# Kernel tuning notes

Measured on AMD Instinct MI355X. Metric: run time of the kernel, lower is better.

The kernel has to match this reference:

```python
import jax, jax.numpy as jnp
import numpy as np

B, T, D = 2, 2048, 1024
NH, DH = 16, 64  # inner = NH*DH = D
SCALE_INIT = 0.02


def setup_inputs() -> dict:
    key = jax.random.key(0)
    kx, kq, kk, kv, ko = jax.random.split(key, 5)
    return {
        "x": jax.random.normal(kx, (B, T, D), dtype=jnp.float32),
        "Wq": jax.random.normal(kq, (D, NH * DH), dtype=jnp.float32) * SCALE_INIT,
        "Wk": jax.random.normal(kk, (D, NH * DH), dtype=jnp.float32) * SCALE_INIT,
        "Wv": jax.random.normal(kv, (D, NH * DH), dtype=jnp.float32) * SCALE_INIT,
        "Wo": jax.random.normal(ko, (NH * DH, D), dtype=jnp.float32) * SCALE_INIT,
    }


def reference(x, Wq, Wk, Wv, Wo):
    # x: (B, T, D)
    b, t, _ = x.shape

    def split_heads(h):
        # (B, T, NH*DH) -> (B, NH, T, DH)
        return h.reshape(b, t, NH, DH).transpose(0, 2, 1, 3)

    q = split_heads(x @ Wq)
    k = split_heads(x @ Wk)
    v = split_heads(x @ Wv)

    scale = jnp.asarray(1.0 / np.sqrt(DH), dtype=x.dtype)
    # The per-chunk loop in the original is mathematically equivalent to
    # full causal attention: each query row attends to keys with k_pos <= q_pos.
    scores = jnp.einsum("bhqd,bhkd->bhqk", q, k) * scale  # (B, NH, T, T)
    causal_mask = jnp.arange(t)[None, :] > jnp.arange(t)[:, None]  # k_pos > q_pos
    scores = jnp.where(causal_mask, -jnp.inf, scores)
    attn = jax.nn.softmax(scores, axis=-1)
    attn = jnp.nan_to_num(attn)  # matches torch.nan_to_num (no fully-masked rows in causal case)
    o = jnp.einsum("bhqk,bhkd->bhqd", attn, v)  # (B, NH, T, DH)
    o = o.transpose(0, 2, 1, 3).reshape(b, t, NH * DH)  # merge heads
    return o @ Wo  # (B, T, D)
```

## Files before the change

### kernel.cpp

```cpp
#include <hip/hip_runtime.h>
#include <hip/hip_bf16.h>
#include <string.h>

#define Bsz 2
#define Tsz 2048
#define Dsz 1024
#define NHsz 16
#define Msz (Bsz*Tsz)

typedef unsigned short bfu;
typedef __attribute__((ext_vector_type(8))) short short8;
typedef __attribute__((ext_vector_type(4))) short short4v;
typedef __attribute__((ext_vector_type(4))) float floatx4;

__device__ __forceinline__ bfu f2bf(float f) {
  unsigned int u = __builtin_bit_cast(unsigned int, f);
  u += 0x7fffu + ((u >> 16) & 1u);
  return (bfu)(u >> 16);
}

__device__ __forceinline__ float fexp2(float x) {
#if __has_builtin(__builtin_amdgcn_exp2f)
  return __builtin_amdgcn_exp2f(x);
#else
  return exp2f(x);
#endif
}

__device__ __forceinline__ short4v pack4bf(float a, float b, float c_, float d) {
  __hip_bfloat162 h01 = __float22bfloat162_rn(make_float2(a, b));
  __hip_bfloat162 h23 = __float22bfloat162_rn(make_float2(c_, d));
  uint2 uu;
  memcpy(&uu.x, &h01, 4);
  memcpy(&uu.y, &h23, 4);
  return __builtin_bit_cast(short4v, uu);
}

__device__ __forceinline__ short8 pack8bf(float4 a, float4 b) {
  __hip_bfloat162 h0 = __float22bfloat162_rn(make_float2(a.x, a.y));
  __hip_bfloat162 h1 = __float22bfloat162_rn(make_float2(a.z, a.w));
  __hip_bfloat162 h2 = __float22bfloat162_rn(make_float2(b.x, b.y));
  __hip_bfloat162 h3 = __float22bfloat162_rn(make_float2(b.z, b.w));
  uint4 u;
  memcpy(&u.x, &h0, 4); memcpy(&u.y, &h1, 4);
  memcpy(&u.z, &h2, 4); memcpy(&u.w, &h3, 4);
  return __builtin_bit_cast(short8, u);
}

__device__ __forceinline__ void async16(const void* g, void* l) {
  void* gnc = (void*)g;
  __builtin_amdgcn_global_load_lds((__attribute__((address_space(1))) void*)gnc,
                                   (__attribute__((address_space(3))) void*)l,
                                   16, 0, 0);
}

__global__ __launch_bounds__(256) void transpose_w(const float* __restrict__ W0, const float* __restrict__ W1,
                                                   const float* __restrict__ W2, const float* __restrict__ W3,
                                                   bfu* __restrict__ wt) {
  __shared__ float tile[32][33];
  const float* W = blockIdx.z == 0 ? W0 : blockIdx.z == 1 ? W1 : blockIdx.z == 2 ? W2 : W3;
  const float s = (blockIdx.z == 0) ? 0.18033688011112042f : 1.0f;
  bfu* WT = wt + (size_t)blockIdx.z * Dsz * Dsz;
  int tx = threadIdx.x, ty = threadIdx.y;
  int kb = blockIdx.y * 32, nb = blockIdx.x * 32;
#pragma unroll
  for (int i = 0; i < 4; ++i)
    tile[ty + i*8][tx] = W[(size_t)(kb + ty + i*8) * Dsz + nb + tx];
  __syncthreads();
#pragma unroll
  for (int i = 0; i < 4; ++i)
    WT[(size_t)(nb + ty + i*8) * Dsz + kb + tx] = f2bf(tile[tx][ty + i*8] * s);
}

template <bool F32OUT, bool AF32, int NT>
__global__ __launch_bounds__(256) void gemm128(const void* __restrict__ Ain, const bfu* __restrict__ Bt0,
                                               void* __restrict__ C0, int K, int N,
                                               size_t strideB, size_t strideC) {
  constexpr int NJ = NT / 32;
  const int tid = threadIdx.x, wave = tid >> 6, lane = tid & 63;
  const int g = lane >> 4, c = lane & 15;
  const int m0 = blockIdx.y * 128, n0 = blockIdx.x * NT;
  const bfu* Bt = Bt0 + strideB * blockIdx.z;
  __shared__ bfu smem[4096 + NT * 32];
  bfu* As = smem;
  bfu* Bs = smem + 4096;
  floatx4 acc[4][NJ] = {};
  const int srow = lane >> 2, scol = (lane & 3) * 8;
  const bfu* gB = Bt + (size_t)(n0 + srow) * K + scol;
  const int wm = (wave >> 1) * 64, wn = (wave & 1) * (NT / 2);

  short8 areg[2];
  if (AF32) {
#pragma unroll
    for (int cc = 0; cc < 2; ++cc) {
      const float* pa = (const float*)Ain +
          (size_t)(m0 + (wave*2 + cc)*16 + srow) * K + scol;
      areg[cc] = pack8bf(((const float4*)pa)[0], ((const float4*)pa)[1]);
    }
  }
  const bfu* gA = AF32 ? nullptr : (const bfu*)Ain + (size_t)(m0 + srow) * K + scol;

  for (int k0 = 0; k0 < K; k0 += 32) {
    __syncthreads();
#pragma unroll
    for (int cc = 0; cc < 2; ++cc) {
      const int chunk = wave * 2 + cc;
      if (AF32) *(short8*)&As[chunk * 512 + lane * 8] = areg[cc];
      else      async16(gA + (size_t)chunk * 16 * K + k0, &As[chunk * 512]);
    }
#pragma unroll
    for (int cc = 0; cc < NT/64; ++cc) {
      const int chunk = wave * (NT/64) + cc;
      async16(gB + (size_t)chunk * 16 * K + k0, &Bs[chunk * 512]);
    }
    __syncthreads();
    if (AF32 && k0 + 32 < K) {
#pragma unroll
      for (int cc = 0; cc < 2; ++cc) {
        const float* pa = (const float*)Ain +
            (size_t)(m0 + (wave*2 + cc)*16 + srow) * K + (k0 + 32) + scol;
        areg[cc] = pack8bf(((const float4*)pa)[0], ((const float4*)pa)[1]);
      }
    }
    short8 afr[4], bfr[NJ];
#pragma unroll
    for (int t = 0; t < 4; ++t) afr[t] = *(const short8*)&As[(wm + t*16 + c) * 32 + g * 8];
#pragma unroll
    for (int t = 0; t < NJ; ++t) bfr[t] = *(const short8*)&Bs[(wn + t*16 + c) * 32 + g * 8];
#pragma unroll
    for (int i = 0; i < 4; ++i)
#pragma unroll
      for (int j = 0; j < NJ; ++j)
        acc[i][j] = __builtin_amdgcn_mfma_f32_16x16x32_bf16(afr[i], bfr[j], acc[i][j], 0, 0, 0);
  }

  const bool vtrans = (!F32OUT) && (NT == 128) && (blockIdx.z == 2);
  if (vtrans) {
    bfu* vtp = (bfu*)C0 + (size_t)2 * strideC;
#pragma unroll
    for (int p = 0; p < 2; ++p) {
      __syncthreads();
      if ((wave & 1) == p) {
#pragma unroll
        for (int i = 0; i < 4; ++i)
#pragma unroll
          for (int j = 0; j < NJ; ++j) {
            const int nl = j*16 + c;
            const int mg = ((wm + i*16) >> 3) + (g >> 1);
            const int phys = nl * 128 + ((mg ^ (nl & 15)) << 3) + ((g & 1) << 2);
            *(short4v*)&smem[phys] = pack4bf(acc[i][j][0], acc[i][j][1],
                                             acc[i][j][2], acc[i][j][3]);
          }
      }
      __syncthreads();
      const int h_ = (n0 + p * 64) >> 6;
      bfu* dst = vtp + ((size_t)((m0 >> 11) * 16 + h_) * 64) * Tsz + (m0 & 2047);
#pragma unroll
      for (int s = 0; s < 4; ++s) {
        const int nl = s * 16 + (tid >> 4);
        const int me = (tid & 15) << 3;
        const int phys = nl * 128 + (((me >> 3) ^ (nl & 15)) << 3);
        *(short8*)&dst[(size_t)nl * Tsz + me] = *(const short8*)&smem[phys];
      }
    }
    return;
  }

#pragma unroll
  for (int i = 0; i < 4; ++i) {
#pragma unroll
    for (int j = 0; j < NJ; ++j) {
      const int m = m0 + wm + i*16 + g*4;
      const int n = n0 + wn + j*16 + c;
#pragma unroll
      for (int r = 0; r < 4; ++r) {
        float v = acc[i][j][r];
        if (F32OUT) ((float*)C0)[(size_t)(m + r) * N + n] = v;
        else        ((bfu*)C0)[strideC * blockIdx.z + (size_t)(m + r) * N + n] = f2bf(v);
      }
    }
  }
}

__global__ __launch_bounds__(256, 4) void attn_kernel(const bfu* __restrict__ qkv,
                                                      bfu* __restrict__ obuf) {
  const int tid = threadIdx.x, wave = tid >> 6, lane = tid & 63;
  const int g = (lane >> 4) & 3, c = lane & 15, c7 = c & 7;

  const int flat = (int)blockIdx.y * 32 + (int)blockIdx.x;
  const int xcd = flat & 7, idx = flat >> 3;
  const int s = idx >> 5, t = idx & 31;
  const int tt = (s & 2) ? ((t + 16) & 31) : t;
  const int j  = (s & 1) ? (31 - tt) : tt;
  const int bh = xcd * 4 + s;
  const int b = bh >> 4, h = bh & 15;

  const size_t hbq = (size_t)b * Tsz * Dsz + h * 64;
  const bfu* Qp = qkv + hbq;
  const bfu* Kp = qkv + (size_t)Msz * Dsz + hbq;
  const bfu* Vt = qkv + (size_t)2 * Msz * Dsz + (size_t)bh * 64 * Tsz;

  __shared__ bfu Ks[2][64 * 64];
  __shared__ bfu Vs[2][64 * 64];

  const int qw = j * 64 + wave * 16;

  short8 bq[2];
#pragma unroll
  for (int kk = 0; kk < 2; ++kk)
    bq[kk] = *(const short8*)(Qp + (size_t)(qw + c) * Dsz + kk * 32 + g * 8);

  const int srow8 = lane >> 3;
  const int soff = ((lane & 7) ^ srow8) << 3;
  const bfu* kpp[2]; const bfu* vpp[2];
#pragma unroll
  for (int cc = 0; cc < 2; ++cc) {
    const int ch = wave * 2 + cc;
    kpp[cc] = Kp + (size_t)(ch * 8 + srow8) * Dsz + soff;
    vpp[cc] = Vt + (size_t)(ch * 8 + srow8) * Tsz + soff;
  }

  floatx4 acc[4] = {};
  float mi = -3.0e38f, li = 0.0f;
  const floatx4 z4 = {0.0f, 0.0f, 0.0f, 0.0f};

#pragma unroll
  for (int cc = 0; cc < 2; ++cc) {
    const int ch = wave * 2 + cc;
    async16(kpp[cc], &Ks[0][ch * 512]);
    async16(vpp[cc], &Vs[0][ch * 512]);
    kpp[cc] += (size_t)64 * Dsz;
    vpp[cc] += 64;
  }

  for (int kt = 0; kt <= j; ++kt) {
    const int cur = kt & 1;
    if (kt < j) {
#pragma unroll
      for (int cc = 0; cc < 2; ++cc) {
        const int ch = wave * 2 + cc;
        async16(kpp[cc], &Ks[cur ^ 1][ch * 512]);
        async16(vpp[cc], &Vs[cur ^ 1][ch * 512]);
        kpp[cc] += (size_t)64 * Dsz;
        vpp[cc] += 64;
      }
      asm volatile("s_waitcnt vmcnt(4)" ::: "memory");
    } else {
      asm volatile("s_waitcnt vmcnt(0)" ::: "memory");
    }
    __builtin_amdgcn_s_barrier();
    asm volatile("" ::: "memory");

    const bfu* KsC = &Ks[cur][0];
    const bfu* VsC = &Vs[cur][0];

    floatx4 st[4];
    __builtin_amdgcn_s_setprio(1);
#pragma unroll
    for (int mk = 0; mk < 4; ++mk) {
      const short8 kf = *(const short8*)&KsC[(mk * 16 + c) * 64 + ((g ^ c7) << 3)];
      st[mk] = __builtin_amdgcn_mfma_f32_16x16x32_bf16(kf, bq[0], z4, 0, 0, 0);
    }
#pragma unroll
    for (int mk = 0; mk < 4; ++mk) {
      const short8 kf = *(const short8*)&KsC[(mk * 16 + c) * 64 + (((4 + g) ^ c7) << 3)];
      st[mk] = __builtin_amdgcn_mfma_f32_16x16x32_bf16(kf, bq[1], st[mk], 0, 0, 0);
    }
    __builtin_amdgcn_s_setprio(0);

    if (kt == j) {
#pragma unroll
      for (int mk = 0; mk < 4; ++mk) {
        const int keyb = kt * 64 + mk * 16 + g * 4;
#pragma unroll
        for (int r = 0; r < 4; ++r)
          if (keyb + r > qw + c) st[mk][r] = -1.0e38f;
      }
    }

    float mloc = -3.0e38f;
#pragma unroll
    for (int mk = 0; mk < 4; ++mk)
      mloc = fmaxf(mloc, fmaxf(fmaxf(st[mk][0], st[mk][1]),
                               fmaxf(st[mk][2], st[mk][3])));
    mloc = fmaxf(mloc, __shfl_xor(mloc, 16));
    mloc = fmaxf(mloc, __shfl_xor(mloc, 32));
    const float mcand = fmaxf(mi, mloc);
    const bool resc = !__all(mcand - mi <= 8.0f);
    const float mnew = resc ? mcand : mi;
    float sum = 0.0f;
    short4v pa[4];
#pragma unroll
    for (int mk = 0; mk < 4; ++mk) {
      const float p0 = fexp2(st[mk][0] - mnew);
      const float p1 = fexp2(st[mk][1] - mnew);
      const float p2 = fexp2(st[mk][2] - mnew);
      const float p3 = fexp2(st[mk][3] - mnew);
      sum += (p0 + p1) + (p2 + p3);
      pa[mk] = pack4bf(p0, p1, p2, p3);
    }
    sum += __shfl_xor(sum, 16);
    sum += __shfl_xor(sum, 32);
    if (resc) {
      const float alpha = fexp2(mi - mnew);
      li = li * alpha + sum;
      mi = mnew;
      float al[4];
#pragma unroll
      for (int r = 0; r < 4; ++r) al[r] = __shfl(alpha, (lane & 48) | (g * 4 + r));
#pragma unroll
      for (int nd = 0; nd < 4; ++nd)
#pragma unroll
        for (int r = 0; r < 4; ++r) acc[nd][r] *= al[r];
    } else {
      li += sum;
    }

    __builtin_amdgcn_s_setprio(1);
#pragma unroll
    for (int mk = 0; mk < 4; ++mk)
#pragma unroll
      for (int nd = 0; nd < 4; ++nd) {
        const short4v vf = *(const short4v*)&VsC[(nd * 16 + c) * 64 +
            ((((mk << 1) + (g >> 1)) ^ c7) << 3) + ((g & 1) << 2)];
        acc[nd] = __builtin_amdgcn_mfma_f32_16x16x16bf16_1k(pa[mk], vf, acc[nd], 0, 0, 0);
      }
    __builtin_amdgcn_s_setprio(0);

    asm volatile("" ::: "memory");
    __builtin_amdgcn_s_barrier();
    asm volatile("" ::: "memory");
  }

#pragma unroll
  for (int r = 0; r < 4; ++r) {
    const float inv = 1.0f / __shfl(li, (lane & 48) | (g * 4 + r));
#pragma unroll
    for (int nd = 0; nd < 4; ++nd)
      obuf[(size_t)(b * Tsz + qw + g * 4 + r) * Dsz + h * 64 + nd * 16 + c] =
          f2bf(acc[nd][r] * inv);
  }
}

extern "C" void kernel_launch(void* const* d_in, const int* in_sizes, int n_in,
                              void* d_out, int out_size, void* d_ws, size_t ws_size,
                              hipStream_t stream) {
  const float* x  = (const float*)d_in[0];
  const float* Wq = (const float*)d_in[1];
  const float* Wk = (const float*)d_in[2];
  const float* Wv = (const float*)d_in[3];
  const float* Wo = (const float*)d_in[4];
  float* out = (float*)d_out;

  bfu* wt   = (bfu*)d_ws;
  bfu* qkv  = wt  + (size_t)4 * Dsz * Dsz;
  bfu* obuf = qkv + (size_t)3 * Msz * Dsz;

  transpose_w<<<dim3(32, 32, 4), dim3(32, 8), 0, stream>>>(Wq, Wk, Wv, Wo, wt);
  gemm128<false, true, 128><<<dim3(Dsz / 128, Msz / 128, 3), dim3(256), 0, stream>>>(
      (const void*)x, wt, (void*)qkv, Dsz, Dsz, (size_t)Dsz * Dsz, (size_t)Msz * Dsz);
  attn_kernel<<<dim3(32, 32), dim3(256), 0, stream>>>(qkv, obuf);
  gemm128<true, false, 64><<<dim3(Dsz / 64, Msz / 128, 1), dim3(256), 0, stream>>>(
      (const void*)obuf, wt + (size_t)3 * Dsz * Dsz, (void*)out, Dsz, Dsz,
      (size_t)0, (size_t)0);
}
```

Measured before the change: 199.3 us.

## Pair causal query tiles per block and defer row-sum reduction

Each attention block now processes two query tiles, j0 and 31-j0, one after the other. This balances causal work per block and halves the grid to 512 blocks, with launch bounds relaxed from 4 to 2 blocks per SIMD. The softmax step no longer does the max cross-lane shuffles unless a rescale is triggered, and it keeps per-lane partial row sums that are reduced once at the end instead of every tile. The trade-off is fewer resident blocks and less parallelism, in exchange for even per-block work and less shuffle overhead.

```diff
diff --git a/kernel.cpp b/kernel.cpp
--- a/kernel.cpp
+++ b/kernel.cpp
@@ -182,16 +182,14 @@
   }
 }
 
-__global__ __launch_bounds__(256, 4) void attn_kernel(const bfu* __restrict__ qkv,
+__global__ __launch_bounds__(256, 2) void attn_kernel(const bfu* __restrict__ qkv,
                                                       bfu* __restrict__ obuf) {
   const int tid = threadIdx.x, wave = tid >> 6, lane = tid & 63;
   const int g = (lane >> 4) & 3, c = lane & 15, c7 = c & 7;
 
-  const int flat = (int)blockIdx.y * 32 + (int)blockIdx.x;
-  const int xcd = flat & 7, idx = flat >> 3;
-  const int s = idx >> 5, t = idx & 31;
-  const int tt = (s & 2) ? ((t + 16) & 31) : t;
-  const int j  = (s & 1) ? (31 - tt) : tt;
+  const int flat = (int)blockIdx.y * 16 + (int)blockIdx.x;
+  const int xcd = flat & 7, r_ = flat >> 3;
+  const int s = r_ & 3, j0 = r_ >> 2;
   const int bh = xcd * 4 + s;
   const int b = bh >> 4, h = bh & 15;
 
@@ -203,142 +201,143 @@
   __shared__ bfu Ks[2][64 * 64];
   __shared__ bfu Vs[2][64 * 64];
 
-  const int qw = j * 64 + wave * 16;
-
-  short8 bq[2];
-#pragma unroll
-  for (int kk = 0; kk < 2; ++kk)
-    bq[kk] = *(const short8*)(Qp + (size_t)(qw + c) * Dsz + kk * 32 + g * 8);
-
   const int srow8 = lane >> 3;
   const int soff = ((lane & 7) ^ srow8) << 3;
-  const bfu* kpp[2]; const bfu* vpp[2];
-#pragma unroll
-  for (int cc = 0; cc < 2; ++cc) {
-    const int ch = wave * 2 + cc;
-    kpp[cc] = Kp + (size_t)(ch * 8 + srow8) * Dsz + soff;
-    vpp[cc] = Vt + (size_t)(ch * 8 + srow8) * Tsz + soff;
-  }
-
-  floatx4 acc[4] = {};
-  float mi = -3.0e38f, li = 0.0f;
   const floatx4 z4 = {0.0f, 0.0f, 0.0f, 0.0f};
 
-#pragma unroll
-  for (int cc = 0; cc < 2; ++cc) {
-    const int ch = wave * 2 + cc;
-    async16(kpp[cc], &Ks[0][ch * 512]);
-    async16(vpp[cc], &Vs[0][ch * 512]);
-    kpp[cc] += (size_t)64 * Dsz;
-    vpp[cc] += 64;
-  }
-
-  for (int kt = 0; kt <= j; ++kt) {
-    const int cur = kt & 1;
-    if (kt < j) {
-#pragma unroll
-      for (int cc = 0; cc < 2; ++cc) {
-        const int ch = wave * 2 + cc;
-        async16(kpp[cc], &Ks[cur ^ 1][ch * 512]);
-        async16(vpp[cc], &Vs[cur ^ 1][ch * 512]);
-        kpp[cc] += (size_t)64 * Dsz;
-        vpp[cc] += 64;
-      }
-      asm volatile("s_waitcnt vmcnt(4)" ::: "memory");
-    } else {
-      asm volatile("s_waitcnt vmcnt(0)" ::: "memory");
-    }
-    __builtin_amdgcn_s_barrier();
-    asm volatile("" ::: "memory");
-
-    const bfu* KsC = &Ks[cur][0];
-    const bfu* VsC = &Vs[cur][0];
-
-    floatx4 st[4];
-    __builtin_amdgcn_s_setprio(1);
-#pragma unroll
-    for (int mk = 0; mk < 4; ++mk) {
-      const short8 kf = *(const short8*)&KsC[(mk * 16 + c) * 64 + ((g ^ c7) << 3)];
-      st[mk] = __builtin_amdgcn_mfma_f32_16x16x32_bf16(kf, bq[0], z4, 0, 0, 0);
-    }
-#pragma unroll
-    for (int mk = 0; mk < 4; ++mk) {
-      const short8 kf = *(const short8*)&KsC[(mk * 16 + c) * 64 + (((4 + g) ^ c7) << 3)];
-      st[mk] = __builtin_amdgcn_mfma_f32_16x16x32_bf16(kf, bq[1], st[mk], 0, 0, 0);
-    }
-    __builtin_amdgcn_s_setprio(0);
-
-    if (kt == j) {
+  for (int hf = 0; hf < 2; ++hf) {
+    const int j = hf ? (31 - j0) : j0;
+    const int qw = j * 64 + wave * 16;
+
+    short8 bq[2];
+#pragma unroll
+    for (int kk = 0; kk < 2; ++kk)
+      bq[kk] = *(const short8*)(Qp + (size_t)(qw + c) * Dsz + kk * 32 + g * 8);
+
+    const bfu* kpp[2]; const bfu* vpp[2];
+#pragma unroll
+    for (int cc = 0; cc < 2; ++cc) {
+      const int ch = wave * 2 + cc;
+      kpp[cc] = Kp + (size_t)(ch * 8 + srow8) * Dsz + soff;
+      vpp[cc] = Vt + (size_t)(ch * 8 + srow8) * Tsz + soff;
+    }
+
+    floatx4 acc[4] = {};
+    float mi = -3.0e38f, li = 0.0f;
+
+#pragma unroll
+    for (int cc = 0; cc < 2; ++cc) {
+      const int ch = wave * 2 + cc;
+      async16(kpp[cc], &Ks[0][ch * 512]);
+      async16(vpp[cc], &Vs[0][ch * 512]);
+      kpp[cc] += (size_t)64 * Dsz;
+      vpp[cc] += 64;
+    }
+
+    for (int kt = 0; kt <= j; ++kt) {
+      const int cur = kt & 1;
+      if (kt < j) {
+#pragma unroll
+        for (int cc = 0; cc < 2; ++cc) {
+          const int ch = wave * 2 + cc;
+          async16(kpp[cc], &Ks[cur ^ 1][ch * 512]);
+          async16(vpp[cc], &Vs[cur ^ 1][ch * 512]);
+          kpp[cc] += (size_t)64 * Dsz;
+          vpp[cc] += 64;
+        }
+        asm volatile("s_waitcnt vmcnt(4)" ::: "memory");
+      } else {
+        asm volatile("s_waitcnt vmcnt(0)" ::: "memory");
+      }
+      __builtin_amdgcn_s_barrier();
+      asm volatile("" ::: "memory");
+
+      const bfu* KsC = &Ks[cur][0];
+      const bfu* VsC = &Vs[cur][0];
+
+      floatx4 st[4];
+      __builtin_amdgcn_s_setprio(1);
 #pragma unroll
       for (int mk = 0; mk < 4; ++mk) {
-        const int keyb = kt * 64 + mk * 16 + g * 4;
-#pragma unroll
-        for (int r = 0; r < 4; ++r)
-          if (keyb + r > qw + c) st[mk][r] = -1.0e38f;
-      }
-    }
-
-    float mloc = -3.0e38f;
-#pragma unroll
-    for (int mk = 0; mk < 4; ++mk)
-      mloc = fmaxf(mloc, fmaxf(fmaxf(st[mk][0], st[mk][1]),
-                               fmaxf(st[mk][2], st[mk][3])));
-    mloc = fmaxf(mloc, __shfl_xor(mloc, 16));
-    mloc = fmaxf(mloc, __shfl_xor(mloc, 32));
-    const float mcand = fmaxf(mi, mloc);
-    const bool resc = !__all(mcand - mi <= 8.0f);
-    const float mnew = resc ? mcand : mi;
-    float sum = 0.0f;
-    short4v pa[4];
-#pragma unroll
-    for (int mk = 0; mk < 4; ++mk) {
-      const float p0 = fexp2(st[mk][0] - mnew);
-      const float p1 = fexp2(st[mk][1] - mnew);
-      const float p2 = fexp2(st[mk][2] - mnew);
-      const float p3 = fexp2(st[mk][3] - mnew);
-      sum += (p0 + p1) + (p2 + p3);
-      pa[mk] = pack4bf(p0, p1, p2, p3);
-    }
-    sum += __shfl_xor(sum, 16);
-    sum += __shfl_xor(sum, 32);
-    if (resc) {
-      const float alpha = fexp2(mi - mnew);
-      li = li * alpha + sum;
-      mi = mnew;
-      float al[4];
-#pragma unroll
-      for (int r = 0; r < 4; ++r) al[r] = __shfl(alpha, (lane & 48) | (g * 4 + r));
+        const short8 kf = *(const short8*)&KsC[(mk * 16 + c) * 64 + ((g ^ c7) << 3)];
+        st[mk] = __builtin_amdgcn_mfma_f32_16x16x32_bf16(kf, bq[0], z4, 0, 0, 0);
+      }
+#pragma unroll
+      for (int mk = 0; mk < 4; ++mk) {
+        const short8 kf = *(const short8*)&KsC[(mk * 16 + c) * 64 + (((4 + g) ^ c7) << 3)];
+        st[mk] = __builtin_amdgcn_mfma_f32_16x16x32_bf16(kf, bq[1], st[mk], 0, 0, 0);
+      }
+      __builtin_amdgcn_s_setprio(0);
+
+      if (kt == j) {
+#pragma unroll
+        for (int mk = 0; mk < 4; ++mk) {
+          const int keyb = kt * 64 + mk * 16 + g * 4;
+#pragma unroll
+          for (int r = 0; r < 4; ++r)
+            if (keyb + r > qw + c) st[mk][r] = -1.0e38f;
+        }
+      }
+
+      float mloc = -3.0e38f;
+#pragma unroll
+      for (int mk = 0; mk < 4; ++mk)
+        mloc = fmaxf(mloc, fmaxf(fmaxf(st[mk][0], st[mk][1]),
+                                 fmaxf(st[mk][2], st[mk][3])));
+      const bool resc = !__all(mloc <= mi + 8.0f);
+      if (resc) {
+        float mr = fmaxf(mloc, __shfl_xor(mloc, 16));
+        mr = fmaxf(mr, __shfl_xor(mr, 32));
+        const float mnew = fmaxf(mi, mr);
+        const float alpha = fexp2(mi - mnew);
+        li *= alpha;
+        mi = mnew;
+        float al[4];
+#pragma unroll
+        for (int rr = 0; rr < 4; ++rr) al[rr] = __shfl(alpha, (lane & 48) | (g * 4 + rr));
+#pragma unroll
+        for (int nd = 0; nd < 4; ++nd)
+#pragma unroll
+          for (int rr = 0; rr < 4; ++rr) acc[nd][rr] *= al[rr];
+      }
+      short4v pa[4];
+#pragma unroll
+      for (int mk = 0; mk < 4; ++mk) {
+        const float p0 = fexp2(st[mk][0] - mi);
+        const float p1 = fexp2(st[mk][1] - mi);
+        const float p2 = fexp2(st[mk][2] - mi);
+        const float p3 = fexp2(st[mk][3] - mi);
+        li += (p0 + p1) + (p2 + p3);
+        pa[mk] = pack4bf(p0, p1, p2, p3);
+      }
+
+      __builtin_amdgcn_s_setprio(1);
+#pragma unroll
+      for (int mk = 0; mk < 4; ++mk)
+#pragma unroll
+        for (int nd = 0; nd < 4; ++nd) {
+          const short4v vf = *(const short4v*)&VsC[(nd * 16 + c) * 64 +
+              ((((mk << 1) + (g >> 1)) ^ c7) << 3) + ((g & 1) << 2)];
+          acc[nd] = __builtin_amdgcn_mfma_f32_16x16x16bf16_1k(pa[mk], vf, acc[nd], 0, 0, 0);
+        }
+      __builtin_amdgcn_s_setprio(0);
+
+      asm volatile("" ::: "memory");
+      __builtin_amdgcn_s_barrier();
+      asm volatile("" ::: "memory");
+    }
+
+    float lt = li;
+    lt += __shfl_xor(lt, 16);
+    lt += __shfl_xor(lt, 32);
+#pragma unroll
+    for (int rr = 0; rr < 4; ++rr) {
+      const float inv = 1.0f / __shfl(lt, (lane & 48) | (g * 4 + rr));
 #pragma unroll
       for (int nd = 0; nd < 4; ++nd)
-#pragma unroll
-        for (int r = 0; r < 4; ++r) acc[nd][r] *= al[r];
-    } else {
-      li += sum;
-    }
-
-    __builtin_amdgcn_s_setprio(1);
-#pragma unroll
-    for (int mk = 0; mk < 4; ++mk)
-#pragma unroll
-      for (int nd = 0; nd < 4; ++nd) {
-        const short4v vf = *(const short4v*)&VsC[(nd * 16 + c) * 64 +
-            ((((mk << 1) + (g >> 1)) ^ c7) << 3) + ((g & 1) << 2)];
-        acc[nd] = __builtin_amdgcn_mfma_f32_16x16x16bf16_1k(pa[mk], vf, acc[nd], 0, 0, 0);
-      }
-    __builtin_amdgcn_s_setprio(0);
-
-    asm volatile("" ::: "memory");
-    __builtin_amdgcn_s_barrier();
-    asm volatile("" ::: "memory");
-  }
-
-#pragma unroll
-  for (int r = 0; r < 4; ++r) {
-    const float inv = 1.0f / __shfl(li, (lane & 48) | (g * 4 + r));
-#pragma unroll
-    for (int nd = 0; nd < 4; ++nd)
-      obuf[(size_t)(b * Tsz + qw + g * 4 + r) * Dsz + h * 64 + nd * 16 + c] =
-          f2bf(acc[nd][r] * inv);
+        obuf[(size_t)(b * Tsz + qw + g * 4 + rr) * Dsz + h * 64 + nd * 16 + c] =
+            f2bf(acc[nd][rr] * inv);
+    }
   }
 }
 
@@ -359,7 +358,7 @@
   transpose_w<<<dim3(32, 32, 4), dim3(32, 8), 0, stream>>>(Wq, Wk, Wv, Wo, wt);
   gemm128<false, true, 128><<<dim3(Dsz / 128, Msz / 128, 3), dim3(256), 0, stream>>>(
       (const void*)x, wt, (void*)qkv, Dsz, Dsz, (size_t)Dsz * Dsz, (size_t)Msz * Dsz);
-  attn_kernel<<<dim3(32, 32), dim3(256), 0, stream>>>(qkv, obuf);
+  attn_kernel<<<dim3(16, 32), dim3(256), 0, stream>>>(qkv, obuf);
   gemm128<true, false, 64><<<dim3(Dsz / 64, Msz / 128, 1), dim3(256), 0, stream>>>(
       (const void*)obuf, wt + (size_t)3 * Dsz * Dsz, (void*)out, Dsz, Dsz,
       (size_t)0, (size_t)0);
```

Result: faster. 193.2 us (-3.1%).
